# Optimization experiments

Hardware: AMD Instinct MI355X
Metric: run time of the kernel (lower is better)

The kernel has to match this reference:

```python
import jax, jax.numpy as jnp
import numpy as np

MAX_NODES = 1024
FEAT = 64
HID = 32
B, S = 32, 4096


def setup_inputs() -> dict:
    key = jax.random.key(0)
    ks = jax.random.split(key, 9)
    flow_features = jax.random.normal(ks[0], (B, S, FEAT), dtype=jnp.float32)
    src_ips = jax.random.randint(ks[1], (B, S), 0, MAX_NODES, dtype=jnp.int32)
    dst_ips = jax.random.randint(ks[2], (B, S), 0, MAX_NODES, dtype=jnp.int32)
    flow_volumes = jax.random.uniform(ks[3], (B, S), dtype=jnp.float32)
    # learned parameters
    node_emb = jax.random.normal(ks[4], (MAX_NODES, FEAT), dtype=jnp.float32)
    W1 = jax.random.normal(ks[5], (2 * FEAT, HID), dtype=jnp.float32) * (1.0 / np.sqrt(2 * FEAT))
    b1 = jnp.zeros((HID,), dtype=jnp.float32)
    W2 = jax.random.normal(ks[6], (HID, 1), dtype=jnp.float32) * (1.0 / np.sqrt(HID))
    b2 = jnp.zeros((1,), dtype=jnp.float32)
    return {"flow_features": flow_features, "src_ips": src_ips, "dst_ips": dst_ips,
            "flow_volumes": flow_volumes, "node_emb": node_emb,
            "W1": W1, "b1": b1, "W2": W2, "b2": b2}


def reference(flow_features, src_ips, dst_ips, flow_volumes, node_emb, W1, b1, W2, b2):
    b_, s_, f_ = flow_features.shape
    n_ = node_emb.shape[0]
    bidx = jnp.arange(b_)[:, None]  # (B,1) broadcast over seq

    # ---- scatter-add flow features into destination nodes ----
    node_features = jnp.zeros((b_, n_, f_), dtype=flow_features.dtype)
    node_features = node_features.at[bidx, dst_ips].add(flow_features)
    # F.normalize(p=2, dim=-1): x / max(||x||, eps)
    norm = jnp.linalg.norm(node_features, axis=-1, keepdims=True)
    node_features = node_features / jnp.maximum(norm, 1e-12)

    # ---- gather embeddings, edge MLP, scatter weights into adjacency ----
    src_e = node_emb[src_ips]  # (B,S,F)
    dst_e = node_emb[dst_ips]  # (B,S,F)
    h = jax.nn.relu(jnp.concatenate([src_e, dst_e], axis=-1) @ W1 + b1)  # (B,S,32)
    edge_w = jax.nn.sigmoid((h @ W2 + b2)[..., 0])  # (B,S)
    vol_w = jax.nn.sigmoid(flow_volumes / 1000.0)
    w = edge_w * vol_w  # (B,S)

    adjacency = jnp.zeros((b_, n_, n_), dtype=flow_features.dtype)
    # semantics up to scatter ordering of colliding edges)
    adjacency = adjacency.at[bidx, src_ips, dst_ips].set(w)
    adjacency = adjacency.at[bidx, dst_ips, src_ips].set(w)
    return node_features, adjacency
```

## Files before the change

kernel.cpp:

```cpp
#include <hip/hip_runtime.h>
#include <cstdint>
#include <cstddef>

#define BB 32
#define SS 4096
#define FEAT_ 64
#define HID_ 32
#define NN 1024
#define RPB 8

__global__ void node_feat_kernel(const float* __restrict__ flow,
                                 const int* __restrict__ dst,
                                 float* __restrict__ nf) {
    int row0 = blockIdx.x << 2;
    int b = row0 >> 10;
    __shared__ int sdst[SS];

    const int4* g = (const int4*)(dst + (size_t)b * SS);
    int4* sd4 = (int4*)sdst;
    for (int i = threadIdx.x; i < SS / 4; i += 256) sd4[i] = g[i];
    __syncthreads();

    int wave = threadIdx.x >> 6;
    int lane = threadIdx.x & 63;
    int node = (row0 + wave) & (NN - 1);
    const float* fb = flow + ((size_t)b * SS << 6);

    float acc = 0.0f;
    for (int s0 = 0; s0 < SS; s0 += 64) {
        int d = sdst[s0 + lane];
        unsigned long long m = __ballot(d == node);
        while (m) {
            int bit = __ffsll((long long)m) - 1;
            m &= m - 1;
            acc += fb[((s0 + bit) << 6) + lane];
        }
    }

    float ss = acc * acc;
    #pragma unroll
    for (int off = 32; off > 0; off >>= 1) ss += __shfl_xor(ss, off, 64);
    float denom = fmaxf(sqrtf(ss), 1e-12f);
    nf[((size_t)(row0 + wave) << 6) + lane] = acc / denom;
}

__global__ void mlp_kernel(const int* __restrict__ src,
                           const int* __restrict__ dst,
                           const float* __restrict__ vol,
                           const float* __restrict__ emb,
                           const float* __restrict__ W1,
                           const float* __restrict__ b1,
                           const float* __restrict__ W2,
                           const float* __restrict__ b2,
                           float* __restrict__ wout) {
    int i = blockIdx.x * blockDim.x + threadIdx.x;
    int si = src[i], di = dst[i];

    float acc[HID_];
    #pragma unroll
    for (int j = 0; j < HID_; ++j) acc[j] = b1[j];

    #pragma unroll
    for (int half = 0; half < 2; ++half) {
        const float* e = emb + ((half ? di : si) << 6);
        const float* w = W1 + half * 64 * HID_;
        for (int k = 0; k < 64; k += 4) {
            float4 v = *(const float4*)(e + k);
            #pragma unroll
            for (int j = 0; j < HID_; ++j) {
                float a = acc[j];
                a += v.x * w[(k + 0) * HID_ + j];
                a += v.y * w[(k + 1) * HID_ + j];
                a += v.z * w[(k + 2) * HID_ + j];
                a += v.w * w[(k + 3) * HID_ + j];
                acc[j] = a;
            }
        }
    }

    float dotv = b2[0];
    #pragma unroll
    for (int j = 0; j < HID_; ++j) dotv += fmaxf(acc[j], 0.0f) * W2[j];
    float edge_w = 1.0f / (1.0f + expf(-dotv));
    float vol_w  = 1.0f / (1.0f + expf(-vol[i] / 1000.0f));
    wout[i] = edge_w * vol_w;
}

__global__ void adj_dense_kernel(const int* __restrict__ src,
                                 const int* __restrict__ dst,
                                 const float* __restrict__ wbuf,
                                 float* __restrict__ adj) {
    int b  = blockIdx.x >> 7;
    int r0 = (blockIdx.x & 127) << 3;
    int tid = threadIdx.x;

    __shared__ int D[RPB * NN];

    int4* D4 = (int4*)D;
    int4 z; z.x = z.y = z.z = z.w = 0;
    #pragma unroll
    for (int i = 0; i < RPB * NN / 4 / 256; ++i) D4[tid + i * 256] = z;
    __syncthreads();

    const int* sb = src + (size_t)b * SS;
    const int* db = dst + (size_t)b * SS;

    for (int s = tid; s < SS; s += 256) {
        int sv = sb[s], dv = db[s];
        unsigned lr1 = (unsigned)(sv - r0);
        if (lr1 < RPB) atomicMax(&D[(lr1 << 10) + dv], s + 1);
        unsigned lr2 = (unsigned)(dv - r0);
        if (lr2 < RPB) atomicMax(&D[(lr2 << 10) + sv], SS + s + 1);
    }
    __syncthreads();

    const float* wb = wbuf + (size_t)b * SS;
    for (int s = tid; s < SS; s += 256) {
        int sv = sb[s], dv = db[s];
        unsigned lr1 = (unsigned)(sv - r0);
        unsigned lr2 = (unsigned)(dv - r0);
        if ((lr1 < RPB) | (lr2 < RPB)) {
            int wbits = __float_as_int(wb[s]);
            if (lr1 < RPB && D[(lr1 << 10) + dv] == s + 1)
                D[(lr1 << 10) + dv] = wbits;
            if (lr2 < RPB && D[(lr2 << 10) + sv] == SS + s + 1)
                D[(lr2 << 10) + sv] = wbits;
        }
    }
    __syncthreads();

    const float4* Df = (const float4*)D;
    float4* out = (float4*)(adj + ((size_t)b * NN + r0) * NN);
    #pragma unroll
    for (int i = 0; i < RPB * NN / 4 / 256; ++i) out[tid + i * 256] = Df[tid + i * 256];
}

extern "C" void kernel_launch(void* const* d_in, const int* in_sizes, int n_in,
                              void* d_out, int out_size, void* d_ws, size_t ws_size,
                              hipStream_t stream) {
    const float* flow = (const float*)d_in[0];
    const int*   src  = (const int*)d_in[1];
    const int*   dst  = (const int*)d_in[2];
    const float* vol  = (const float*)d_in[3];
    const float* emb  = (const float*)d_in[4];
    const float* W1   = (const float*)d_in[5];
    const float* b1   = (const float*)d_in[6];
    const float* W2   = (const float*)d_in[7];
    const float* b2   = (const float*)d_in[8];

    float* nf  = (float*)d_out;
    float* adj = nf + (size_t)BB * NN * FEAT_;
    float* wbuf = (float*)d_ws;

    mlp_kernel<<<(BB * SS) / 256, 256, 0, stream>>>(src, dst, vol, emb,
                                                    W1, b1, W2, b2, wbuf);
    adj_dense_kernel<<<BB * (NN / RPB), 256, 0, stream>>>(src, dst, wbuf, adj);
    node_feat_kernel<<<(BB * NN) / 4, 256, 0, stream>>>(flow, dst, nf);
}
```

Baseline: 274.9 us.

## Process four nodes per wave, register-cache indices, use nontemporal stores

```diff
diff --git a/kernel.cpp b/kernel.cpp
--- a/kernel.cpp
+++ b/kernel.cpp
@@ -9,10 +9,12 @@
 #define NN 1024
 #define RPB 8
 
+typedef int v4i __attribute__((ext_vector_type(4)));
+
 __global__ void node_feat_kernel(const float* __restrict__ flow,
                                  const int* __restrict__ dst,
                                  float* __restrict__ nf) {
-    int row0 = blockIdx.x << 2;
+    int row0 = blockIdx.x << 4;
     int b = row0 >> 10;
     __shared__ int sdst[SS];
 
@@ -23,25 +25,32 @@
 
     int wave = threadIdx.x >> 6;
     int lane = threadIdx.x & 63;
-    int node = (row0 + wave) & (NN - 1);
+    int r0 = row0 + (wave << 2);
+    int node0 = r0 & (NN - 1);
     const float* fb = flow + ((size_t)b * SS << 6);
 
-    float acc = 0.0f;
+    float acc[4] = {0.f, 0.f, 0.f, 0.f};
     for (int s0 = 0; s0 < SS; s0 += 64) {
         int d = sdst[s0 + lane];
-        unsigned long long m = __ballot(d == node);
-        while (m) {
-            int bit = __ffsll((long long)m) - 1;
-            m &= m - 1;
-            acc += fb[((s0 + bit) << 6) + lane];
+        #pragma unroll
+        for (int j = 0; j < 4; ++j) {
+            unsigned long long m = __ballot(d == node0 + j);
+            while (m) {
+                int bit = __ffsll((long long)m) - 1;
+                m &= m - 1;
+                acc[j] += fb[((s0 + bit) << 6) + lane];
+            }
         }
     }
 
-    float ss = acc * acc;
     #pragma unroll
-    for (int off = 32; off > 0; off >>= 1) ss += __shfl_xor(ss, off, 64);
-    float denom = fmaxf(sqrtf(ss), 1e-12f);
-    nf[((size_t)(row0 + wave) << 6) + lane] = acc / denom;
+    for (int j = 0; j < 4; ++j) {
+        float ss = acc[j] * acc[j];
+        #pragma unroll
+        for (int off = 32; off > 0; off >>= 1) ss += __shfl_xor(ss, off, 64);
+        float v = acc[j] / fmaxf(sqrtf(ss), 1e-12f);
+        __builtin_nontemporal_store(v, &nf[((size_t)(r0 + j) << 6) + lane]);
+    }
 }
 
 __global__ void mlp_kernel(const int* __restrict__ src,
@@ -96,43 +105,52 @@
 
     __shared__ int D[RPB * NN];
 
+    const int* sb = src + (size_t)b * SS;
+    const int* db = dst + (size_t)b * SS;
+    int svr[16], dvr[16];
+    #pragma unroll
+    for (int i = 0; i < 16; ++i) {
+        svr[i] = sb[tid + (i << 8)];
+        dvr[i] = db[tid + (i << 8)];
+    }
+
     int4* D4 = (int4*)D;
     int4 z; z.x = z.y = z.z = z.w = 0;
     #pragma unroll
     for (int i = 0; i < RPB * NN / 4 / 256; ++i) D4[tid + i * 256] = z;
     __syncthreads();
 
-    const int* sb = src + (size_t)b * SS;
-    const int* db = dst + (size_t)b * SS;
-
-    for (int s = tid; s < SS; s += 256) {
-        int sv = sb[s], dv = db[s];
-        unsigned lr1 = (unsigned)(sv - r0);
-        if (lr1 < RPB) atomicMax(&D[(lr1 << 10) + dv], s + 1);
-        unsigned lr2 = (unsigned)(dv - r0);
-        if (lr2 < RPB) atomicMax(&D[(lr2 << 10) + sv], SS + s + 1);
+    #pragma unroll
+    for (int i = 0; i < 16; ++i) {
+        int s = tid + (i << 8);
+        unsigned lr1 = (unsigned)(svr[i] - r0);
+        if (lr1 < RPB) atomicMax(&D[(lr1 << 10) + dvr[i]], s + 1);
+        unsigned lr2 = (unsigned)(dvr[i] - r0);
+        if (lr2 < RPB) atomicMax(&D[(lr2 << 10) + svr[i]], SS + s + 1);
     }
     __syncthreads();
 
     const float* wb = wbuf + (size_t)b * SS;
-    for (int s = tid; s < SS; s += 256) {
-        int sv = sb[s], dv = db[s];
-        unsigned lr1 = (unsigned)(sv - r0);
-        unsigned lr2 = (unsigned)(dv - r0);
+    #pragma unroll
+    for (int i = 0; i < 16; ++i) {
+        int s = tid + (i << 8);
+        unsigned lr1 = (unsigned)(svr[i] - r0);
+        unsigned lr2 = (unsigned)(dvr[i] - r0);
         if ((lr1 < RPB) | (lr2 < RPB)) {
             int wbits = __float_as_int(wb[s]);
-            if (lr1 < RPB && D[(lr1 << 10) + dv] == s + 1)
-                D[(lr1 << 10) + dv] = wbits;
-            if (lr2 < RPB && D[(lr2 << 10) + sv] == SS + s + 1)
-                D[(lr2 << 10) + sv] = wbits;
+            if (lr1 < RPB && D[(lr1 << 10) + dvr[i]] == s + 1)
+                D[(lr1 << 10) + dvr[i]] = wbits;
+            if (lr2 < RPB && D[(lr2 << 10) + svr[i]] == SS + s + 1)
+                D[(lr2 << 10) + svr[i]] = wbits;
         }
     }
     __syncthreads();
 
-    const float4* Df = (const float4*)D;
-    float4* out = (float4*)(adj + ((size_t)b * NN + r0) * NN);
+    const v4i* Df = (const v4i*)D;
+    v4i* out = (v4i*)(adj + ((size_t)b * NN + r0) * NN);
     #pragma unroll
-    for (int i = 0; i < RPB * NN / 4 / 256; ++i) out[tid + i * 256] = Df[tid + i * 256];
+    for (int i = 0; i < RPB * NN / 4 / 256; ++i)
+        __builtin_nontemporal_store(Df[tid + i * 256], &out[tid + i * 256]);
 }
 
 extern "C" void kernel_launch(void* const* d_in, const int* in_sizes, int n_in,
@@ -155,5 +173,5 @@
     mlp_kernel<<<(BB * SS) / 256, 256, 0, stream>>>(src, dst, vol, emb,
                                                     W1, b1, W2, b2, wbuf);
     adj_dense_kernel<<<BB * (NN / RPB), 256, 0, stream>>>(src, dst, wbuf, adj);
-    node_feat_kernel<<<(BB * NN) / 4, 256, 0, stream>>>(flow, dst, nf);
+    node_feat_kernel<<<(BB * NN) / 16, 256, 0, stream>>>(flow, dst, nf);
 }
```

Result: faster. 242.0 us (-12.0%).
